# Optimization experiments

Hardware: AMD Instinct MI355X
Metric: run time of the kernel (lower is better)

Reference implementation:

```python
import jax, jax.numpy as jnp
import numpy as np

N = 100000
D = 100
E = 1600000


def setup_inputs() -> dict:
    key = jax.random.key(0)
    k1, k2, k3, k4 = jax.random.split(key, 4)
    embedding = jax.random.normal(k1, (N, D), dtype=jnp.float32)
    adj_rows = jax.random.randint(k2, (E,), 0, N, dtype=jnp.int32)
    adj_cols = jax.random.randint(k3, (E,), 0, N, dtype=jnp.int32)
    adj_vals = jax.random.uniform(k4, (E,), dtype=jnp.float32)
    return {
        "embedding": embedding,
        "adj_rows": adj_rows,
        "adj_cols": adj_cols,
        "adj_vals": adj_vals,
        "layer_num": 3,
    }


def _spmm(rows, cols, vals, x):
    # sparse [N,N] @ dense [N,D] via gather + weighted segment-sum scatter
    msgs = x[cols] * vals[:, None]           # [E, D]
    return jax.ops.segment_sum(msgs, rows, num_segments=N)  # [N, D]


def reference(embedding, adj_rows, adj_cols, adj_vals, layer_num):
    # out = sum_{i=0}^{layer_num} A^i x  (accumulate hops, including layer 0)
    h = embedding
    acc = embedding
    for _ in range(layer_num):
        h = _spmm(adj_rows, adj_cols, adj_vals, h)
        acc = acc + h
    return acc
```

## Files before the change

kernel.cpp:

```cpp
#include <hip/hip_runtime.h>


#define NODES 100000
#define DIM 100
#define DIM4 25
#define CH 13
#define BSHIFT 8
#define NBUCKETS ((NODES + 255) >> 8)
#define P1_BLOCKS 256

typedef _Float16 half4_t __attribute__((ext_vector_type(4)));
typedef _Float16 half8_t __attribute__((ext_vector_type(8)));

__global__ void cvt_pad_kernel(const float4* __restrict__ src, half4_t* __restrict__ dst) {
    int i = blockIdx.x * blockDim.x + threadIdx.x;
    if (i >= NODES * 26) return;
    int row = i / 26, c = i - row * 26;
    half4_t h;
    if (c < 25) {
        float4 f = src[row * 25 + c];
        h.x = (_Float16)f.x; h.y = (_Float16)f.y; h.z = (_Float16)f.z; h.w = (_Float16)f.w;
    } else {
        h.x = (_Float16)0.f; h.y = (_Float16)0.f; h.z = (_Float16)0.f; h.w = (_Float16)0.f;
    }
    dst[row * 26 + c] = h;
}

__global__ void bucket_hist_kernel(const int* __restrict__ rows, int* __restrict__ bktCount, int E) {
    __shared__ int h[NBUCKETS];
    for (int i = threadIdx.x; i < NBUCKETS; i += blockDim.x) h[i] = 0;
    __syncthreads();
    for (int e = blockIdx.x * blockDim.x + threadIdx.x; e < E; e += gridDim.x * blockDim.x)
        atomicAdd(&h[rows[e] >> BSHIFT], 1);
    __syncthreads();
    for (int i = threadIdx.x; i < NBUCKETS; i += blockDim.x)
        if (h[i]) atomicAdd(&bktCount[i], h[i]);
}

__global__ void bucket_scan_kernel(const int* __restrict__ bktCount,
                                   int* __restrict__ bktStart, int* __restrict__ bktCur) {
    __shared__ int s[512];
    int tid = threadIdx.x;
    int v = (tid < NBUCKETS) ? bktCount[tid] : 0;
    s[tid] = v;
    __syncthreads();
    for (int off = 1; off < 512; off <<= 1) {
        int t = (tid >= off) ? s[tid - off] : 0;
        __syncthreads();
        s[tid] += t;
        __syncthreads();
    }
    int excl = s[tid] - v;
    if (tid <= NBUCKETS) bktStart[tid] = excl;
    if (tid < NBUCKETS)  bktCur[tid]  = excl;
}

__global__ void pass1_kernel(const int* __restrict__ rows, const int* __restrict__ cols,
                             const float* __restrict__ vals,
                             int* __restrict__ bktCur, int2* __restrict__ staging, int E) {
    __shared__ int cnt[NBUCKETS];
    __shared__ int base[NBUCKETS];
    int tid = threadIdx.x;
    for (int i = tid; i < NBUCKETS; i += blockDim.x) cnt[i] = 0;
    __syncthreads();
    int chunk = (E + gridDim.x - 1) / gridDim.x;
    int s = blockIdx.x * chunk;
    int e = min(E, s + chunk);
    for (int i = s + tid; i < e; i += blockDim.x)
        atomicAdd(&cnt[rows[i] >> BSHIFT], 1);
    __syncthreads();
    for (int i = tid; i < NBUCKETS; i += blockDim.x) {
        int c = cnt[i];
        base[i] = c ? atomicAdd(&bktCur[i], c) : 0;
        cnt[i] = 0;
    }
    __syncthreads();
    for (int i = s + tid; i < e; i += blockDim.x) {
        int r = rows[i];
        int b = r >> BSHIFT;
        int pos = base[b] + atomicAdd(&cnt[b], 1);
        staging[pos] = make_int2(cols[i] | ((r & 255) << 17), __float_as_int(vals[i]));
    }
}

__global__ void pass2_kernel(const int* __restrict__ bktStart, const int2* __restrict__ staging,
                             int* __restrict__ rowstart, int2* __restrict__ csr) {
    __shared__ int hist[256];
    __shared__ int sc[256];
    __shared__ int cur[256];
    int b = blockIdx.x, tid = threadIdx.x;
    int s = bktStart[b], e = bktStart[b + 1];
    hist[tid] = 0;
    __syncthreads();
    for (int i = s + tid; i < e; i += blockDim.x)
        atomicAdd(&hist[(staging[i].x >> 17) & 255], 1);
    __syncthreads();
    int v = hist[tid];
    sc[tid] = v;
    __syncthreads();
    for (int off = 1; off < 256; off <<= 1) {
        int t = (tid >= off) ? sc[tid - off] : 0;
        __syncthreads();
        sc[tid] += t;
        __syncthreads();
    }
    int excl = sc[tid] - v;
    rowstart[(b << BSHIFT) + tid] = s + excl;
    cur[tid] = excl;
    __syncthreads();
    for (int i = s + tid; i < e; i += blockDim.x) {
        int2 rec = staging[i];
        int lr = (rec.x >> 17) & 255;
        int pos = atomicAdd(&cur[lr], 1);
        csr[s + pos] = make_int2(rec.x & 0x1FFFF, rec.y);
    }
}

__global__ void gather_mid_kernel(const int* __restrict__ rowstart,
                                  const int2* __restrict__ csr,
                                  const half8_t* __restrict__ x,
                                  half8_t* __restrict__ h) {
    int gid = blockIdx.x * blockDim.x + threadIdx.x;
    int row = gid >> 4, lane = gid & 15;
    if (row >= NODES || lane >= CH) return;
    int s = rowstart[row], e = rowstart[row + 1];
    float acc[8] = {0.f, 0.f, 0.f, 0.f, 0.f, 0.f, 0.f, 0.f};
    int i = s;
    for (; i + 1 < e; i += 2) {
        int2 r0 = csr[i], r1 = csr[i + 1];
        half8_t a = x[(size_t)r0.x * CH + lane];
        half8_t b = x[(size_t)r1.x * CH + lane];
        float v0 = __int_as_float(r0.y), v1 = __int_as_float(r1.y);
        #pragma unroll
        for (int k = 0; k < 8; ++k) acc[k] += v0 * (float)a[k] + v1 * (float)b[k];
    }
    if (i < e) {
        int2 r0 = csr[i];
        half8_t a = x[(size_t)r0.x * CH + lane];
        float v0 = __int_as_float(r0.y);
        #pragma unroll
        for (int k = 0; k < 8; ++k) acc[k] += v0 * (float)a[k];
    }
    half8_t hv;
    #pragma unroll
    for (int k = 0; k < 8; ++k) hv[k] = (_Float16)acc[k];
    h[(size_t)row * CH + lane] = hv;
}

__global__ void gather_last_kernel(const int* __restrict__ rowstart,
                                   const int2* __restrict__ csr,
                                   const half8_t* __restrict__ x,
                                   const half8_t* __restrict__ h1,
                                   const half8_t* __restrict__ h2,
                                   const float4* __restrict__ emb,
                                   float4* __restrict__ out) {
    int gid = blockIdx.x * blockDim.x + threadIdx.x;
    int row = gid >> 4, lane = gid & 15;
    if (row >= NODES || lane >= CH) return;
    int s = rowstart[row], e = rowstart[row + 1];
    float acc[8] = {0.f, 0.f, 0.f, 0.f, 0.f, 0.f, 0.f, 0.f};
    int i = s;
    for (; i + 1 < e; i += 2) {
        int2 r0 = csr[i], r1 = csr[i + 1];
        half8_t a = x[(size_t)r0.x * CH + lane];
        half8_t b = x[(size_t)r1.x * CH + lane];
        float v0 = __int_as_float(r0.y), v1 = __int_as_float(r1.y);
        #pragma unroll
        for (int k = 0; k < 8; ++k) acc[k] += v0 * (float)a[k] + v1 * (float)b[k];
    }
    if (i < e) {
        int2 r0 = csr[i];
        half8_t a = x[(size_t)r0.x * CH + lane];
        float v0 = __int_as_float(r0.y);
        #pragma unroll
        for (int k = 0; k < 8; ++k) acc[k] += v0 * (float)a[k];
    }
    size_t pidx = (size_t)row * CH + lane;
    half8_t a1 = h1[pidx], a2 = h2[pidx];
    int f4 = row * DIM4 + lane * 2;
    float4 o0 = emb[f4];
    o0.x += acc[0] + (float)a1[0] + (float)a2[0];
    o0.y += acc[1] + (float)a1[1] + (float)a2[1];
    o0.z += acc[2] + (float)a1[2] + (float)a2[2];
    o0.w += acc[3] + (float)a1[3] + (float)a2[3];
    out[f4] = o0;
    if (lane < 12) {
        float4 o1 = emb[f4 + 1];
        o1.x += acc[4] + (float)a1[4] + (float)a2[4];
        o1.y += acc[5] + (float)a1[5] + (float)a2[5];
        o1.z += acc[6] + (float)a1[6] + (float)a2[6];
        o1.w += acc[7] + (float)a1[7] + (float)a2[7];
        out[f4 + 1] = o1;
    }
}

extern "C" void kernel_launch(void* const* d_in, const int* in_sizes, int n_in,
                              void* d_out, int out_size, void* d_ws, size_t ws_size,
                              hipStream_t stream) {
    const float* emb  = (const float*)d_in[0];
    const int*   rows = (const int*)  d_in[1];
    const int*   cols = (const int*)  d_in[2];
    const float* vals = (const float*)d_in[3];
    const int E = in_sizes[1];

    const size_t ndp_bytes = (size_t)NODES * 104 * sizeof(_Float16);

    char* w = (char*)d_ws;
    half8_t* x0p      = (half8_t*)w;  w += ndp_bytes;
    half8_t* h1p      = (half8_t*)w;  w += ndp_bytes;
    half8_t* h2p      = (half8_t*)w;  w += ndp_bytes;
    int2*    staging  = (int2*)   w;  w += (size_t)E * sizeof(int2);
    int2*    csr      = (int2*)   w;  w += (size_t)E * sizeof(int2);
    int*     rowstart = (int*)    w;  w += (size_t)(NBUCKETS << BSHIFT) * sizeof(int);
    int*     bktCount = (int*)    w;  w += 512 * sizeof(int);
    int*     bktStart = (int*)    w;  w += 512 * sizeof(int);
    int*     bktCur   = (int*)    w;  w += 512 * sizeof(int);

    float4* out = (float4*)d_out;

    hipMemsetAsync(bktCount, 0, NBUCKETS * sizeof(int), stream);
    cvt_pad_kernel<<<(NODES * 26 + 255) / 256, 256, 0, stream>>>((const float4*)emb, (half4_t*)x0p);
    bucket_hist_kernel<<<P1_BLOCKS, 256, 0, stream>>>(rows, bktCount, E);
    bucket_scan_kernel<<<1, 512, 0, stream>>>(bktCount, bktStart, bktCur);
    pass1_kernel<<<P1_BLOCKS, 256, 0, stream>>>(rows, cols, vals, bktCur, staging, E);
    pass2_kernel<<<NBUCKETS, 256, 0, stream>>>(bktStart, staging, rowstart, csr);

    const long long threads = (long long)NODES * 16;
    dim3 gGrid((unsigned)((threads + 255) / 256)), gBlock(256);
    gather_mid_kernel<<<gGrid, gBlock, 0, stream>>>(rowstart, csr, x0p, h1p);
    gather_mid_kernel<<<gGrid, gBlock, 0, stream>>>(rowstart, csr, h1p, h2p);
    gather_last_kernel<<<gGrid, gBlock, 0, stream>>>(rowstart, csr, h2p, h1p, h2p,
                                                     (const float4*)emb, out);
}
```

Before: 395.3 us.

## Sort CSR edges by column tile within rows, fuse convert with histogram, unroll gather

The CSR build now sorts edges inside each row by column tile (col >> 13) using a 4096-bin histogram per bucket, so neighbour gathers within a row are grouped by column region, which may help cache locality. The fp16 convert/pad kernel is fused into the bucket histogram kernel to save a launch, and the gather loops are unrolled by 4 to keep more loads in flight. The larger shared histogram and the per-thread 16-entry scan add cost to pass2, and the sort only orders edges inside a row, which has about 16 edges on average here.

```diff
diff --git a/kernel.cpp b/kernel.cpp
--- a/kernel.cpp
+++ b/kernel.cpp
@@ -7,30 +7,34 @@
 #define CH 13
 #define BSHIFT 8
 #define NBUCKETS ((NODES + 255) >> 8)
-#define P1_BLOCKS 256
+#define NPAD (NBUCKETS << BSHIFT)
+#define TILESHIFT 13
+#define NBINS 4096
 
 typedef _Float16 half4_t __attribute__((ext_vector_type(4)));
 typedef _Float16 half8_t __attribute__((ext_vector_type(8)));
 
-__global__ void cvt_pad_kernel(const float4* __restrict__ src, half4_t* __restrict__ dst) {
-    int i = blockIdx.x * blockDim.x + threadIdx.x;
-    if (i >= NODES * 26) return;
-    int row = i / 26, c = i - row * 26;
-    half4_t h;
-    if (c < 25) {
-        float4 f = src[row * 25 + c];
-        h.x = (_Float16)f.x; h.y = (_Float16)f.y; h.z = (_Float16)f.z; h.w = (_Float16)f.w;
-    } else {
-        h.x = (_Float16)0.f; h.y = (_Float16)0.f; h.z = (_Float16)0.f; h.w = (_Float16)0.f;
-    }
-    dst[row * 26 + c] = h;
-}
-
-__global__ void bucket_hist_kernel(const int* __restrict__ rows, int* __restrict__ bktCount, int E) {
+__global__ void cvt_hist_kernel(const float4* __restrict__ emb, half4_t* __restrict__ x0,
+                                const int* __restrict__ rows, int* __restrict__ bktCount, int E) {
     __shared__ int h[NBUCKETS];
     for (int i = threadIdx.x; i < NBUCKETS; i += blockDim.x) h[i] = 0;
     __syncthreads();
-    for (int e = blockIdx.x * blockDim.x + threadIdx.x; e < E; e += gridDim.x * blockDim.x)
+    int stride = gridDim.x * blockDim.x;
+    int gid = blockIdx.x * blockDim.x + threadIdx.x;
+    for (int i = gid; i < NODES * 26; i += stride) {
+        int r = i / 26, c = i - r * 26;
+        half4_t hv;
+        if (c < 25) {
+            float4 f = emb[r * 25 + c];
+            hv.x = (_Float16)f.x; hv.y = (_Float16)f.y;
+            hv.z = (_Float16)f.z; hv.w = (_Float16)f.w;
+        } else {
+            hv.x = (_Float16)0.f; hv.y = (_Float16)0.f;
+            hv.z = (_Float16)0.f; hv.w = (_Float16)0.f;
+        }
+        x0[i] = hv;
+    }
+    for (int e = gid; e < E; e += stride)
         atomicAdd(&h[rows[e] >> BSHIFT], 1);
     __syncthreads();
     for (int i = threadIdx.x; i < NBUCKETS; i += blockDim.x)
@@ -85,34 +89,40 @@
 
 __global__ void pass2_kernel(const int* __restrict__ bktStart, const int2* __restrict__ staging,
                              int* __restrict__ rowstart, int2* __restrict__ csr) {
-    __shared__ int hist[256];
-    __shared__ int sc[256];
-    __shared__ int cur[256];
-    int b = blockIdx.x, tid = threadIdx.x;
+    __shared__ int hist[NBINS];
+    __shared__ int psum[256];
+    int b = blockIdx.x, t = threadIdx.x;
     int s = bktStart[b], e = bktStart[b + 1];
-    hist[tid] = 0;
-    __syncthreads();
-    for (int i = s + tid; i < e; i += blockDim.x)
-        atomicAdd(&hist[(staging[i].x >> 17) & 255], 1);
-    __syncthreads();
-    int v = hist[tid];
-    sc[tid] = v;
+    for (int i = t; i < NBINS; i += 256) hist[i] = 0;
+    __syncthreads();
+    for (int i = s + t; i < e; i += 256) {
+        int key = staging[i].x;
+        int bin = (((key >> 17) & 255) << 4) | ((key & 0x1FFFF) >> TILESHIFT);
+        atomicAdd(&hist[bin], 1);
+    }
+    __syncthreads();
+    int loc[16];
+    int run = 0;
+    #pragma unroll
+    for (int j = 0; j < 16; ++j) { loc[j] = run; run += hist[t * 16 + j]; }
+    psum[t] = run;
     __syncthreads();
     for (int off = 1; off < 256; off <<= 1) {
-        int t = (tid >= off) ? sc[tid - off] : 0;
-        __syncthreads();
-        sc[tid] += t;
-        __syncthreads();
-    }
-    int excl = sc[tid] - v;
-    rowstart[(b << BSHIFT) + tid] = s + excl;
-    cur[tid] = excl;
-    __syncthreads();
-    for (int i = s + tid; i < e; i += blockDim.x) {
+        int x = (t >= off) ? psum[t - off] : 0;
+        __syncthreads();
+        psum[t] += x;
+        __syncthreads();
+    }
+    int base = psum[t] - run;
+    rowstart[(b << BSHIFT) + t] = s + base;
+    #pragma unroll
+    for (int j = 0; j < 16; ++j) hist[t * 16 + j] = base + loc[j];
+    __syncthreads();
+    for (int i = s + t; i < e; i += 256) {
         int2 rec = staging[i];
-        int lr = (rec.x >> 17) & 255;
-        int pos = atomicAdd(&cur[lr], 1);
-        csr[s + pos] = make_int2(rec.x & 0x1FFFF, rec.y);
+        int bin = (((rec.x >> 17) & 255) << 4) | ((rec.x & 0x1FFFF) >> TILESHIFT);
+        int p = atomicAdd(&hist[bin], 1);
+        csr[s + p] = make_int2(rec.x & 0x1FFFF, rec.y);
     }
 }
 
@@ -126,20 +136,25 @@
     int s = rowstart[row], e = rowstart[row + 1];
     float acc[8] = {0.f, 0.f, 0.f, 0.f, 0.f, 0.f, 0.f, 0.f};
     int i = s;
-    for (; i + 1 < e; i += 2) {
-        int2 r0 = csr[i], r1 = csr[i + 1];
-        half8_t a = x[(size_t)r0.x * CH + lane];
-        half8_t b = x[(size_t)r1.x * CH + lane];
+    for (; i + 3 < e; i += 4) {
+        int2 r0 = csr[i], r1 = csr[i + 1], r2 = csr[i + 2], r3 = csr[i + 3];
+        half8_t a0 = x[(size_t)r0.x * CH + lane];
+        half8_t a1 = x[(size_t)r1.x * CH + lane];
+        half8_t a2 = x[(size_t)r2.x * CH + lane];
+        half8_t a3 = x[(size_t)r3.x * CH + lane];
         float v0 = __int_as_float(r0.y), v1 = __int_as_float(r1.y);
-        #pragma unroll
-        for (int k = 0; k < 8; ++k) acc[k] += v0 * (float)a[k] + v1 * (float)b[k];
-    }
-    if (i < e) {
+        float v2 = __int_as_float(r2.y), v3 = __int_as_float(r3.y);
+        #pragma unroll
+        for (int k = 0; k < 8; ++k)
+            acc[k] += v0 * (float)a0[k] + v1 * (float)a1[k]
+                    + v2 * (float)a2[k] + v3 * (float)a3[k];
+    }
+    for (; i < e; ++i) {
         int2 r0 = csr[i];
-        half8_t a = x[(size_t)r0.x * CH + lane];
+        half8_t a0 = x[(size_t)r0.x * CH + lane];
         float v0 = __int_as_float(r0.y);
         #pragma unroll
-        for (int k = 0; k < 8; ++k) acc[k] += v0 * (float)a[k];
+        for (int k = 0; k < 8; ++k) acc[k] += v0 * (float)a0[k];
     }
     half8_t hv;
     #pragma unroll
@@ -160,20 +175,25 @@
     int s = rowstart[row], e = rowstart[row + 1];
     float acc[8] = {0.f, 0.f, 0.f, 0.f, 0.f, 0.f, 0.f, 0.f};
     int i = s;
-    for (; i + 1 < e; i += 2) {
-        int2 r0 = csr[i], r1 = csr[i + 1];
-        half8_t a = x[(size_t)r0.x * CH + lane];
-        half8_t b = x[(size_t)r1.x * CH + lane];
+    for (; i + 3 < e; i += 4) {
+        int2 r0 = csr[i], r1 = csr[i + 1], r2 = csr[i + 2], r3 = csr[i + 3];
+        half8_t a0 = x[(size_t)r0.x * CH + lane];
+        half8_t a1 = x[(size_t)r1.x * CH + lane];
+        half8_t a2 = x[(size_t)r2.x * CH + lane];
+        half8_t a3 = x[(size_t)r3.x * CH + lane];
         float v0 = __int_as_float(r0.y), v1 = __int_as_float(r1.y);
-        #pragma unroll
-        for (int k = 0; k < 8; ++k) acc[k] += v0 * (float)a[k] + v1 * (float)b[k];
-    }
-    if (i < e) {
+        float v2 = __int_as_float(r2.y), v3 = __int_as_float(r3.y);
+        #pragma unroll
+        for (int k = 0; k < 8; ++k)
+            acc[k] += v0 * (float)a0[k] + v1 * (float)a1[k]
+                    + v2 * (float)a2[k] + v3 * (float)a3[k];
+    }
+    for (; i < e; ++i) {
         int2 r0 = csr[i];
-        half8_t a = x[(size_t)r0.x * CH + lane];
+        half8_t a0 = x[(size_t)r0.x * CH + lane];
         float v0 = __int_as_float(r0.y);
         #pragma unroll
-        for (int k = 0; k < 8; ++k) acc[k] += v0 * (float)a[k];
+        for (int k = 0; k < 8; ++k) acc[k] += v0 * (float)a0[k];
     }
     size_t pidx = (size_t)row * CH + lane;
     half8_t a1 = h1[pidx], a2 = h2[pidx];
@@ -211,7 +231,7 @@
     half8_t* h2p      = (half8_t*)w;  w += ndp_bytes;
     int2*    staging  = (int2*)   w;  w += (size_t)E * sizeof(int2);
     int2*    csr      = (int2*)   w;  w += (size_t)E * sizeof(int2);
-    int*     rowstart = (int*)    w;  w += (size_t)(NBUCKETS << BSHIFT) * sizeof(int);
+    int*     rowstart = (int*)    w;  w += (size_t)(NPAD + 256) * sizeof(int);
     int*     bktCount = (int*)    w;  w += 512 * sizeof(int);
     int*     bktStart = (int*)    w;  w += 512 * sizeof(int);
     int*     bktCur   = (int*)    w;  w += 512 * sizeof(int);
@@ -219,10 +239,10 @@
     float4* out = (float4*)d_out;
 
     hipMemsetAsync(bktCount, 0, NBUCKETS * sizeof(int), stream);
-    cvt_pad_kernel<<<(NODES * 26 + 255) / 256, 256, 0, stream>>>((const float4*)emb, (half4_t*)x0p);
-    bucket_hist_kernel<<<P1_BLOCKS, 256, 0, stream>>>(rows, bktCount, E);
+    cvt_hist_kernel<<<1024, 256, 0, stream>>>((const float4*)emb, (half4_t*)x0p,
+                                              rows, bktCount, E);
     bucket_scan_kernel<<<1, 512, 0, stream>>>(bktCount, bktStart, bktCur);
-    pass1_kernel<<<P1_BLOCKS, 256, 0, stream>>>(rows, cols, vals, bktCur, staging, E);
+    pass1_kernel<<<256, 256, 0, stream>>>(rows, cols, vals, bktCur, staging, E);
     pass2_kernel<<<NBUCKETS, 256, 0, stream>>>(bktStart, staging, rowstart, csr);
 
     const long long threads = (long long)NODES * 16;
```

New measurement: 394.9 us. About the same (-0.1%).
